# Kernel tuning notes

Hardware: AMD Instinct MI355X
Metric: run time of the kernel (lower is better)

Reference implementation:

```python
import jax, jax.numpy as jnp
import numpy as np

DIM, HID, E, K = 1024, 2048, 8, 2


def setup_inputs() -> dict:
    key = jax.random.key(0)
    ks = jax.random.split(key, 5)
    x = jax.random.normal(ks[0], (2, 2048, DIM), dtype=jnp.float32)
    # router (torch zero-inits; use small random so routing is non-degenerate)
    router_w = jax.random.normal(ks[1], (DIM, E), dtype=jnp.float32) * 0.02
    router_b = jnp.zeros((E,), dtype=jnp.float32)
    # stacked expert params: w12 [E, dim, 2*hidden], w3 [E, hidden, dim]
    w12 = jax.random.normal(ks[2], (E, DIM, 2 * HID), dtype=jnp.float32) * 0.02
    w3 = jax.random.normal(ks[3], (E, HID, DIM), dtype=jnp.float32) * 0.02
    return {"x": x, "router_w": router_w, "router_b": router_b, "w12": w12, "w3": w3}


def reference(x, router_w, router_b, w12, w3):
    # router logits [b, s, e]; eval mode -> no jitter noise
    logits = jnp.einsum("bsd,de->bse", x, router_w) + router_b
    scores = jax.nn.sigmoid(logits)
    top_v, top_i = jax.lax.top_k(scores, K)            # [b, s, k]
    rw = top_v / (jnp.sum(top_v, axis=-1, keepdims=True) + 1e-6)
    # per-token combine weight for each expert (0 if not routed)
    oh = jax.nn.one_hot(top_i, E, dtype=x.dtype)       # [b, s, k, e]
    cw = jnp.einsum("bsk,bske->bse", rw, oh)           # [b, s, e]
    # dense all-expert SwiGLU (matches original masked-dense math)
    x12 = jnp.einsum("bsd,edh->bseh", x, w12)          # [b, s, e, 2H]
    x1, x2 = jnp.split(x12, 2, axis=-1)
    h = jax.nn.silu(x1) * x2                           # [b, s, e, H]
    eout = jnp.einsum("bseh,ehd->bsed", h, w3)         # [b, s, e, dim]
    out = jnp.einsum("bsed,bse->bsd", eout, cw)
    aux_loss = 0.01 * jnp.mean(logits ** 2)
    return out, aux_loss
```

## Files before the change

### kernel.cpp

```cpp
#include <hip/hip_runtime.h>
#include <hip/hip_bf16.h>
#include <stdint.h>

typedef __bf16 bf16_t;
typedef __bf16 bf16x8 __attribute__((ext_vector_type(8)));
typedef __bf16 bf16x4 __attribute__((ext_vector_type(4)));
typedef float f32x4 __attribute__((ext_vector_type(4)));

#define T_TOK 4096
#define DIM   1024
#define HID   2048
#define NE    8
#define MAXT  72

__device__ __forceinline__ void gload_lds16(const void* g, void* l) {
  __builtin_amdgcn_global_load_lds(
      (const __attribute__((address_space(1))) unsigned int*)g,
      (__attribute__((address_space(3))) unsigned int*)l, 16, 0, 0);
}

__global__ __launch_bounds__(256) void k_wt(const float* __restrict__ in,
                                            bf16_t* __restrict__ out,
                                            int K, int N) {
  __shared__ float tile[64][65];
  const size_t eoff = (size_t)blockIdx.z * K * N;
  const int k0 = blockIdx.y * 64, n0 = blockIdx.x * 64;
  const int tid = threadIdx.x;
#pragma unroll
  for (int it = 0; it < 4; ++it) {
    int k = (tid >> 4) + it * 16;
    int n = (tid & 15) * 4;
    float4 v = *(const float4*)(in + eoff + (size_t)(k0 + k) * N + n0 + n);
    tile[k][n] = v.x; tile[k][n + 1] = v.y; tile[k][n + 2] = v.z; tile[k][n + 3] = v.w;
  }
  __syncthreads();
#pragma unroll
  for (int it = 0; it < 2; ++it) {
    int n = (tid >> 3) + it * 32;
    int kc = (tid & 7) * 8;
    bf16x8 o;
#pragma unroll
    for (int j = 0; j < 8; ++j) o[j] = (bf16_t)tile[kc + j][n];
    *(bf16x8*)(out + eoff + (size_t)(n0 + n) * K + k0 + kc) = o;
  }
}

__global__ __launch_bounds__(256) void k_router(const float* __restrict__ x,
    const float* __restrict__ rw, const float* __restrict__ rb,
    int* __restrict__ counts, int* __restrict__ top_i, float* __restrict__ top_w,
    float* __restrict__ aux, bf16_t* __restrict__ xb) {
  int t = blockIdx.x * 4 + (threadIdx.x >> 6);
  int lane = threadIdx.x & 63;
  const float* xt = x + (size_t)t * DIM;
  float acc[8] = {0.f,0.f,0.f,0.f,0.f,0.f,0.f,0.f};
#pragma unroll
  for (int it = 0; it < 4; ++it) {
    int i = (it * 64 + lane) * 4;
    float4 xv = *(const float4*)(xt + i);
    bf16x4 o;
    o[0] = (bf16_t)xv.x; o[1] = (bf16_t)xv.y; o[2] = (bf16_t)xv.z; o[3] = (bf16_t)xv.w;
    *(bf16x4*)(xb + (size_t)t * DIM + i) = o;
#pragma unroll
    for (int c = 0; c < 4; ++c) {
      float v = (c == 0) ? xv.x : (c == 1) ? xv.y : (c == 2) ? xv.z : xv.w;
      float4 r0 = *(const float4*)(rw + (size_t)(i + c) * 8);
      float4 r1 = *(const float4*)(rw + (size_t)(i + c) * 8 + 4);
      acc[0] += v * r0.x; acc[1] += v * r0.y; acc[2] += v * r0.z; acc[3] += v * r0.w;
      acc[4] += v * r1.x; acc[5] += v * r1.y; acc[6] += v * r1.z; acc[7] += v * r1.w;
    }
  }
#pragma unroll
  for (int m = 32; m >= 1; m >>= 1) {
#pragma unroll
    for (int e = 0; e < 8; ++e) acc[e] += __shfl_xor(acc[e], m, 64);
  }
  if (lane == 0) {
    float s[8]; float sumsq = 0.f;
#pragma unroll
    for (int e = 0; e < 8; ++e) {
      float lg = acc[e] + rb[e];
      sumsq += lg * lg;
      s[e] = 1.f / (1.f + __expf(-lg));
    }
    int i1 = 0;
#pragma unroll
    for (int e = 1; e < 8; ++e) if (s[e] > s[i1]) i1 = e;
    int i2 = (i1 == 0) ? 1 : 0;
#pragma unroll
    for (int e = 0; e < 8; ++e) if (e != i1 && s[e] > s[i2]) i2 = e;
    float v1 = s[i1], v2 = s[i2];
    float den = v1 + v2 + 1e-6f;
    top_i[2 * t]     = i1; top_i[2 * t + 1] = i2;
    top_w[2 * t]     = v1 / den;
    top_w[2 * t + 1] = v2 / den;
    atomicAdd(&counts[i1], 1);
    atomicAdd(&counts[i2], 1);
    atomicAdd(aux, 0.01f * sumsq * (1.f / 32768.f));
  }
}

__global__ void k_plan(const int* __restrict__ counts, int* __restrict__ base,
                       int* __restrict__ tile_e, int* __restrict__ tile_m0) {
  if (threadIdx.x == 0) {
    int s = 0, nt = 0;
    for (int e = 0; e < NE; ++e) {
      base[e] = s;
      int c = counts[e];
      for (int m0 = 0; m0 < c; m0 += 128) { tile_e[nt] = e; tile_m0[nt] = m0; ++nt; }
      s += c;
    }
    for (; nt < MAXT; ++nt) tile_e[nt] = -1;
  }
}

__global__ __launch_bounds__(256) void k_gather(const int* __restrict__ top_i,
    const float* __restrict__ top_w, const int* __restrict__ base,
    int* __restrict__ fill, int* __restrict__ slot_token, float* __restrict__ slot_wt,
    int* __restrict__ slot_of) {
  int t = blockIdx.x * 256 + threadIdx.x;
  if (t >= T_TOK) return;
#pragma unroll
  for (int j = 0; j < 2; ++j) {
    int e = top_i[2 * t + j];
    int p = atomicAdd(&fill[e], 1);
    int g = base[e] + p;
    slot_token[g] = t;
    slot_wt[g]    = top_w[2 * t + j];
    slot_of[2 * t + j] = g;
  }
}

__global__ __launch_bounds__(256) void k_gemm1(
    const bf16_t* __restrict__ xb, const bf16_t* __restrict__ w12t,
    const int* __restrict__ counts, const int* __restrict__ base,
    const int* __restrict__ tile_e, const int* __restrict__ tile_m0,
    const int* __restrict__ slot_token, bf16_t* __restrict__ h) {
  const int e = tile_e[blockIdx.y];
  if (e < 0) return;
  const int m0  = tile_m0[blockIdx.y];
  const int cnt = counts[e];
  const int bas = base[e];
  const int n0 = blockIdx.x * 64;
  const bf16_t* W1 = w12t + (size_t)e * (4096u * 1024u) + (size_t)n0 * 1024u;
  const bf16_t* W2 = W1 + (size_t)2048 * 1024;

  __shared__ bf16_t sA[2][128 * 64];
  __shared__ bf16_t sB1[2][64 * 64];
  __shared__ bf16_t sB2[2][64 * 64];

  const int tid = threadIdx.x, lane = tid & 63, wid = tid >> 6;
  const int wr = wid >> 1, wc = wid & 1;
  const int lr = lane >> 3, sw = (lane & 7) ^ lr;

  int tokA[4];
#pragma unroll
  for (int i = 0; i < 4; ++i) {
    int row = m0 + wid * 32 + i * 8 + lr;
    tokA[i] = slot_token[bas + (row < cnt ? row : cnt - 1)];
  }

  auto stage = [&](int p, int k0) {
#pragma unroll
    for (int i = 0; i < 4; ++i)
      gload_lds16(xb + (size_t)tokA[i] * DIM + k0 + sw * 8,
                  &sA[p][(wid * 32 + i * 8) * 64]);
#pragma unroll
    for (int i = 0; i < 2; ++i) {
      int n = wid * 16 + i * 8 + lr;
      gload_lds16(W1 + (size_t)n * 1024 + k0 + sw * 8, &sB1[p][(wid * 16 + i * 8) * 64]);
      gload_lds16(W2 + (size_t)n * 1024 + k0 + sw * 8, &sB2[p][(wid * 16 + i * 8) * 64]);
    }
  };

  f32x4 acc1[4][2] = {};
  f32x4 acc2[4][2] = {};

  stage(0, 0);
  stage(1, 64);

  const int NT = DIM / 64;
  for (int t = 0; t < NT; ++t) {
    const int p = t & 1;
    if (t + 2 < NT) asm volatile("s_waitcnt vmcnt(8)" ::: "memory");
    else            asm volatile("s_waitcnt vmcnt(0)" ::: "memory");
    __builtin_amdgcn_s_barrier();
    asm volatile("" ::: "memory");
#pragma unroll
    for (int kk = 0; kk < 2; ++kk) {
      const int g = kk * 4 + (lane >> 4);
      bf16x8 a[4], b1[2], b2[2];
#pragma unroll
      for (int mf = 0; mf < 4; ++mf) {
        int r = wr * 64 + mf * 16 + (lane & 15);
        a[mf] = *(const bf16x8*)(&sA[p][r * 64 + ((g ^ (r & 7)) << 3)]);
      }
#pragma unroll
      for (int nf = 0; nf < 2; ++nf) {
        int n = wc * 32 + nf * 16 + (lane & 15);
        b1[nf] = *(const bf16x8*)(&sB1[p][n * 64 + ((g ^ (n & 7)) << 3)]);
        b2[nf] = *(const bf16x8*)(&sB2[p][n * 64 + ((g ^ (n & 7)) << 3)]);
      }
#pragma unroll
      for (int mf = 0; mf < 4; ++mf)
#pragma unroll
        for (int nf = 0; nf < 2; ++nf) {
          acc1[mf][nf] = __builtin_amdgcn_mfma_f32_16x16x32_bf16(a[mf], b1[nf], acc1[mf][nf], 0, 0, 0);
          acc2[mf][nf] = __builtin_amdgcn_mfma_f32_16x16x32_bf16(a[mf], b2[nf], acc2[mf][nf], 0, 0, 0);
        }
    }
    __builtin_amdgcn_sched_barrier(0);
    __builtin_amdgcn_s_barrier();
    asm volatile("" ::: "memory");
    if (t + 2 < NT) stage(p, (t + 2) * 64);
  }

#pragma unroll
  for (int mf = 0; mf < 4; ++mf)
#pragma unroll
    for (int r = 0; r < 4; ++r) {
      int m = wr * 64 + mf * 16 + ((lane >> 4) << 2) + r;
      if (m0 + m < cnt) {
        size_t rowoff = (size_t)(bas + m0 + m) * HID + n0;
#pragma unroll
        for (int nf = 0; nf < 2; ++nf) {
          int col = wc * 32 + nf * 16 + (lane & 15);
          float d1 = acc1[mf][nf][r], d2 = acc2[mf][nf][r];
          h[rowoff + col] = (bf16_t)((d1 / (1.f + __expf(-d1))) * d2);
        }
      }
    }
}

__global__ __launch_bounds__(256) void k_gemm2(
    const bf16_t* __restrict__ h, const bf16_t* __restrict__ w3t,
    const int* __restrict__ counts, const int* __restrict__ base,
    const int* __restrict__ tile_e, const int* __restrict__ tile_m0,
    const float* __restrict__ slot_wt, bf16_t* __restrict__ eout) {
  const int e = tile_e[blockIdx.y];
  if (e < 0) return;
  const int m0  = tile_m0[blockIdx.y];
  const int cnt = counts[e];
  const int bas = base[e];
  const int n0 = blockIdx.x * 128;
  const bf16_t* W = w3t + (size_t)e * (1024u * 2048u);

  __shared__ bf16_t sA[2][128 * 64];
  __shared__ bf16_t sB[2][128 * 64];

  const int tid = threadIdx.x, lane = tid & 63, wid = tid >> 6;
  const int wr = wid >> 1, wc = wid & 1;
  const int lr = lane >> 3, sw = (lane & 7) ^ lr;

  int rowA[4];
#pragma unroll
  for (int i = 0; i < 4; ++i) {
    int row = m0 + wid * 32 + i * 8 + lr;
    rowA[i] = bas + (row < cnt ? row : cnt - 1);
  }

  auto stage = [&](int p, int k0) {
#pragma unroll
    for (int i = 0; i < 4; ++i) {
      int rr = wid * 32 + i * 8;
      gload_lds16(h + (size_t)rowA[i] * HID + k0 + sw * 8, &sA[p][rr * 64]);
      gload_lds16(W + (size_t)(n0 + rr + lr) * 2048 + k0 + sw * 8, &sB[p][rr * 64]);
    }
  };

  f32x4 acc[4][4] = {};

  stage(0, 0);
  stage(1, 64);

  const int NT = HID / 64;
  for (int t = 0; t < NT; ++t) {
    const int p = t & 1;
    if (t + 2 < NT) asm volatile("s_waitcnt vmcnt(8)" ::: "memory");
    else            asm volatile("s_waitcnt vmcnt(0)" ::: "memory");
    __builtin_amdgcn_s_barrier();
    asm volatile("" ::: "memory");
#pragma unroll
    for (int kk = 0; kk < 2; ++kk) {
      const int g = kk * 4 + (lane >> 4);
      bf16x8 a[4], b[4];
#pragma unroll
      for (int mf = 0; mf < 4; ++mf) {
        int r = wr * 64 + mf * 16 + (lane & 15);
        a[mf] = *(const bf16x8*)(&sA[p][r * 64 + ((g ^ (r & 7)) << 3)]);
      }
#pragma unroll
      for (int nf = 0; nf < 4; ++nf) {
        int n = wc * 64 + nf * 16 + (lane & 15);
        b[nf] = *(const bf16x8*)(&sB[p][n * 64 + ((g ^ (n & 7)) << 3)]);
      }
#pragma unroll
      for (int mf = 0; mf < 4; ++mf)
#pragma unroll
        for (int nf = 0; nf < 4; ++nf)
          acc[mf][nf] = __builtin_amdgcn_mfma_f32_16x16x32_bf16(a[mf], b[nf], acc[mf][nf], 0, 0, 0);
    }
    __builtin_amdgcn_sched_barrier(0);
    __builtin_amdgcn_s_barrier();
    asm volatile("" ::: "memory");
    if (t + 2 < NT) stage(p, (t + 2) * 64);
  }

#pragma unroll
  for (int mf = 0; mf < 4; ++mf)
#pragma unroll
    for (int r = 0; r < 4; ++r) {
      int m = wr * 64 + mf * 16 + ((lane >> 4) << 2) + r;
      if (m0 + m < cnt) {
        int gs = bas + m0 + m;
        float wt = slot_wt[gs];
        size_t o = (size_t)gs * DIM + n0;
#pragma unroll
        for (int nf = 0; nf < 4; ++nf) {
          int col = wc * 64 + nf * 16 + (lane & 15);
          eout[o + col] = (bf16_t)(acc[mf][nf][r] * wt);
        }
      }
    }
}

__global__ __launch_bounds__(256) void k_combine(const bf16_t* __restrict__ eout,
    const int* __restrict__ slot_of, float* __restrict__ out) {
  const int t = blockIdx.x;
  const int c = threadIdx.x * 4;
  const int g0 = slot_of[2 * t], g1 = slot_of[2 * t + 1];
  bf16x4 a = *(const bf16x4*)(eout + (size_t)g0 * DIM + c);
  bf16x4 b = *(const bf16x4*)(eout + (size_t)g1 * DIM + c);
  float4 o;
  o.x = (float)a[0] + (float)b[0];
  o.y = (float)a[1] + (float)b[1];
  o.z = (float)a[2] + (float)b[2];
  o.w = (float)a[3] + (float)b[3];
  *(float4*)(out + (size_t)t * DIM + c) = o;
}

extern "C" void kernel_launch(void* const* d_in, const int* in_sizes, int n_in,
                              void* d_out, int out_size, void* d_ws, size_t ws_size,
                              hipStream_t stream) {
  const float* x   = (const float*)d_in[0];
  const float* rw  = (const float*)d_in[1];
  const float* rb  = (const float*)d_in[2];
  const float* w12 = (const float*)d_in[3];
  const float* w3  = (const float*)d_in[4];
  float* out = (float*)d_out;
  float* aux = out + (size_t)T_TOK * DIM;

  char* ws = (char*)d_ws;
  int*   counts     = (int*)(ws + 0);
  int*   fill       = (int*)(ws + 64);
  int*   base       = (int*)(ws + 128);
  int*   top_i      = (int*)(ws + 4096);
  float* top_w      = (float*)(ws + 4096 + 32768);
  int*   slot_token = (int*)(ws + 4096 + 65536);
  float* slot_wt    = (float*)(ws + 4096 + 98304);
  int*   slot_of    = (int*)(ws + 4096 + 131072);
  int*   tile_e     = (int*)(ws + 4096 + 163840);
  int*   tile_m0    = (int*)(ws + 4096 + 164352);
  bf16_t* xb        = (bf16_t*)(ws + 262144);
  bf16_t* h         = (bf16_t*)(ws + 262144 + 8388608);
  bf16_t* wT        = (bf16_t*)(ws + 262144 + 8388608 + 33554432);
  bf16_t* eout      = (bf16_t*)((char*)wT + 33554432);

  hipMemsetAsync(ws, 0, 256, stream);
  hipMemsetAsync(aux, 0, sizeof(float), stream);

  k_wt<<<dim3(64, 16, NE), dim3(256), 0, stream>>>(w12, wT, DIM, 2 * HID);
  k_router<<<dim3(T_TOK / 4), dim3(256), 0, stream>>>(x, rw, rb, counts, top_i, top_w,
                                                      aux, xb);
  k_plan<<<dim3(1), dim3(64), 0, stream>>>(counts, base, tile_e, tile_m0);
  k_gather<<<dim3(T_TOK / 256), dim3(256), 0, stream>>>(top_i, top_w, base, fill,
                                                        slot_token, slot_wt, slot_of);
  k_gemm1<<<dim3(HID / 64, MAXT), dim3(256), 0, stream>>>(
      xb, wT, counts, base, tile_e, tile_m0, slot_token, h);
  k_wt<<<dim3(16, 32, NE), dim3(256), 0, stream>>>(w3, wT, HID, DIM);
  k_gemm2<<<dim3(DIM / 128, MAXT), dim3(256), 0, stream>>>(
      h, wT, counts, base, tile_e, tile_m0, slot_wt, eout);
  k_combine<<<dim3(T_TOK), dim3(256), 0, stream>>>(eout, slot_of, out);
}
```

Before: 382.1 us.

## Switch expert GEMMs to 32x32x16 MFMA, add setprio and column-block remap

Both grouped expert GEMMs now use the 32x32x16 bf16 MFMA instead of 16x16x32. This halves the LDS fragment reads per MFMA and lowers instruction count, and the epilogues are rewritten for the 32x32 accumulator layout. The MFMA section is wrapped in s_setprio, and gemm1 remaps blockIdx.x to a permuted column block order, presumably to improve weight-tile cache locality. The permutation assumes a grid width of 32 and the new fragment layout must match the swizzle, so both are correctness risks.

```diff
diff --git a/kernel.cpp b/kernel.cpp
--- a/kernel.cpp
+++ b/kernel.cpp
@@ -6,6 +6,7 @@
 typedef __bf16 bf16x8 __attribute__((ext_vector_type(8)));
 typedef __bf16 bf16x4 __attribute__((ext_vector_type(4)));
 typedef float f32x4 __attribute__((ext_vector_type(4)));
+typedef float f32x16 __attribute__((ext_vector_type(16)));
 
 #define T_TOK 4096
 #define DIM   1024
@@ -140,7 +141,8 @@
   const int m0  = tile_m0[blockIdx.y];
   const int cnt = counts[e];
   const int bas = base[e];
-  const int n0 = blockIdx.x * 64;
+  const int bx  = blockIdx.x;
+  const int n0  = (((bx & 7) << 2) + (bx >> 3)) << 6;
   const bf16_t* W1 = w12t + (size_t)e * (4096u * 1024u) + (size_t)n0 * 1024u;
   const bf16_t* W2 = W1 + (size_t)2048 * 1024;
 
@@ -172,8 +174,8 @@
     }
   };
 
-  f32x4 acc1[4][2] = {};
-  f32x4 acc2[4][2] = {};
+  f32x16 acc1[2] = {};
+  f32x16 acc2[2] = {};
 
   stage(0, 0);
   stage(1, 64);
@@ -185,29 +187,28 @@
     else            asm volatile("s_waitcnt vmcnt(0)" ::: "memory");
     __builtin_amdgcn_s_barrier();
     asm volatile("" ::: "memory");
-#pragma unroll
-    for (int kk = 0; kk < 2; ++kk) {
-      const int g = kk * 4 + (lane >> 4);
-      bf16x8 a[4], b1[2], b2[2];
-#pragma unroll
-      for (int mf = 0; mf < 4; ++mf) {
-        int r = wr * 64 + mf * 16 + (lane & 15);
-        a[mf] = *(const bf16x8*)(&sA[p][r * 64 + ((g ^ (r & 7)) << 3)]);
-      }
-#pragma unroll
-      for (int nf = 0; nf < 2; ++nf) {
-        int n = wc * 32 + nf * 16 + (lane & 15);
-        b1[nf] = *(const bf16x8*)(&sB1[p][n * 64 + ((g ^ (n & 7)) << 3)]);
-        b2[nf] = *(const bf16x8*)(&sB2[p][n * 64 + ((g ^ (n & 7)) << 3)]);
-      }
-#pragma unroll
-      for (int mf = 0; mf < 4; ++mf)
-#pragma unroll
-        for (int nf = 0; nf < 2; ++nf) {
-          acc1[mf][nf] = __builtin_amdgcn_mfma_f32_16x16x32_bf16(a[mf], b1[nf], acc1[mf][nf], 0, 0, 0);
-          acc2[mf][nf] = __builtin_amdgcn_mfma_f32_16x16x32_bf16(a[mf], b2[nf], acc2[mf][nf], 0, 0, 0);
-        }
-    }
+    __builtin_amdgcn_s_setprio(1);
+#pragma unroll
+    for (int s = 0; s < 4; ++s) {
+      const int c = s * 2 + (lane >> 5);
+      bf16x8 a[2], b1, b2;
+#pragma unroll
+      for (int mf = 0; mf < 2; ++mf) {
+        int r = wr * 64 + mf * 32 + (lane & 31);
+        a[mf] = *(const bf16x8*)(&sA[p][r * 64 + ((c ^ (r & 7)) << 3)]);
+      }
+      {
+        int n = wc * 32 + (lane & 31);
+        b1 = *(const bf16x8*)(&sB1[p][n * 64 + ((c ^ (n & 7)) << 3)]);
+        b2 = *(const bf16x8*)(&sB2[p][n * 64 + ((c ^ (n & 7)) << 3)]);
+      }
+#pragma unroll
+      for (int mf = 0; mf < 2; ++mf) {
+        acc1[mf] = __builtin_amdgcn_mfma_f32_32x32x16_bf16(a[mf], b1, acc1[mf], 0, 0, 0);
+        acc2[mf] = __builtin_amdgcn_mfma_f32_32x32x16_bf16(a[mf], b2, acc2[mf], 0, 0, 0);
+      }
+    }
+    __builtin_amdgcn_s_setprio(0);
     __builtin_amdgcn_sched_barrier(0);
     __builtin_amdgcn_s_barrier();
     asm volatile("" ::: "memory");
@@ -215,18 +216,16 @@
   }
 
 #pragma unroll
-  for (int mf = 0; mf < 4; ++mf)
-#pragma unroll
-    for (int r = 0; r < 4; ++r) {
-      int m = wr * 64 + mf * 16 + ((lane >> 4) << 2) + r;
+  for (int mf = 0; mf < 2; ++mf)
+#pragma unroll
+    for (int reg = 0; reg < 16; ++reg) {
+      int row = (reg & 3) + 8 * (reg >> 2) + 4 * (lane >> 5);
+      int m = wr * 64 + mf * 32 + row;
       if (m0 + m < cnt) {
-        size_t rowoff = (size_t)(bas + m0 + m) * HID + n0;
-#pragma unroll
-        for (int nf = 0; nf < 2; ++nf) {
-          int col = wc * 32 + nf * 16 + (lane & 15);
-          float d1 = acc1[mf][nf][r], d2 = acc2[mf][nf][r];
-          h[rowoff + col] = (bf16_t)((d1 / (1.f + __expf(-d1))) * d2);
-        }
+        int col = wc * 32 + (lane & 31);
+        float d1 = acc1[mf][reg], d2 = acc2[mf][reg];
+        h[(size_t)(bas + m0 + m) * HID + n0 + col] =
+            (bf16_t)((d1 / (1.f + __expf(-d1))) * d2);
       }
     }
 }
@@ -267,7 +266,7 @@
     }
   };
 
-  f32x4 acc[4][4] = {};
+  f32x16 acc[2][2] = {};
 
   stage(0, 0);
   stage(1, 64);
@@ -279,26 +278,28 @@
     else            asm volatile("s_waitcnt vmcnt(0)" ::: "memory");
     __builtin_amdgcn_s_barrier();
     asm volatile("" ::: "memory");
-#pragma unroll
-    for (int kk = 0; kk < 2; ++kk) {
-      const int g = kk * 4 + (lane >> 4);
-      bf16x8 a[4], b[4];
-#pragma unroll
-      for (int mf = 0; mf < 4; ++mf) {
-        int r = wr * 64 + mf * 16 + (lane & 15);
-        a[mf] = *(const bf16x8*)(&sA[p][r * 64 + ((g ^ (r & 7)) << 3)]);
-      }
-#pragma unroll
-      for (int nf = 0; nf < 4; ++nf) {
-        int n = wc * 64 + nf * 16 + (lane & 15);
-        b[nf] = *(const bf16x8*)(&sB[p][n * 64 + ((g ^ (n & 7)) << 3)]);
-      }
-#pragma unroll
-      for (int mf = 0; mf < 4; ++mf)
-#pragma unroll
-        for (int nf = 0; nf < 4; ++nf)
-          acc[mf][nf] = __builtin_amdgcn_mfma_f32_16x16x32_bf16(a[mf], b[nf], acc[mf][nf], 0, 0, 0);
-    }
+    __builtin_amdgcn_s_setprio(1);
+#pragma unroll
+    for (int s = 0; s < 4; ++s) {
+      const int c = s * 2 + (lane >> 5);
+      bf16x8 a[2], b[2];
+#pragma unroll
+      for (int mf = 0; mf < 2; ++mf) {
+        int r = wr * 64 + mf * 32 + (lane & 31);
+        a[mf] = *(const bf16x8*)(&sA[p][r * 64 + ((c ^ (r & 7)) << 3)]);
+      }
+#pragma unroll
+      for (int nf = 0; nf < 2; ++nf) {
+        int n = wc * 64 + nf * 32 + (lane & 31);
+        b[nf] = *(const bf16x8*)(&sB[p][n * 64 + ((c ^ (n & 7)) << 3)]);
+      }
+#pragma unroll
+      for (int mf = 0; mf < 2; ++mf)
+#pragma unroll
+        for (int nf = 0; nf < 2; ++nf)
+          acc[mf][nf] = __builtin_amdgcn_mfma_f32_32x32x16_bf16(a[mf], b[nf], acc[mf][nf], 0, 0, 0);
+    }
+    __builtin_amdgcn_s_setprio(0);
     __builtin_amdgcn_sched_barrier(0);
     __builtin_amdgcn_s_barrier();
     asm volatile("" ::: "memory");
@@ -306,18 +307,19 @@
   }
 
 #pragma unroll
-  for (int mf = 0; mf < 4; ++mf)
-#pragma unroll
-    for (int r = 0; r < 4; ++r) {
-      int m = wr * 64 + mf * 16 + ((lane >> 4) << 2) + r;
+  for (int mf = 0; mf < 2; ++mf)
+#pragma unroll
+    for (int reg = 0; reg < 16; ++reg) {
+      int row = (reg & 3) + 8 * (reg >> 2) + 4 * (lane >> 5);
+      int m = wr * 64 + mf * 32 + row;
       if (m0 + m < cnt) {
         int gs = bas + m0 + m;
         float wt = slot_wt[gs];
         size_t o = (size_t)gs * DIM + n0;
 #pragma unroll
-        for (int nf = 0; nf < 4; ++nf) {
-          int col = wc * 64 + nf * 16 + (lane & 15);
-          eout[o + col] = (bf16_t)(acc[mf][nf][r] * wt);
+        for (int nf = 0; nf < 2; ++nf) {
+          int col = wc * 64 + nf * 32 + (lane & 31);
+          eout[o + col] = (bf16_t)(acc[mf][nf][reg] * wt);
         }
       }
     }
```

Result: slower. 396.2 us (+3.7%).
